# Optimization experiments

Hardware: AMD Instinct MI355X
Metric: run time of the kernel (lower is better)

## Reference

```python
import jax, jax.numpy as jnp
import numpy as np

B, Q, KV = 4, 256, 1024
QS, KS, H, VS = 128, 128, 128, 256

def setup_inputs() -> dict:
    key = jax.random.key(0)
    ks = jax.random.split(key, 7)
    return {
        "queries": jax.random.normal(ks[0], (B, Q, QS), dtype=jnp.float32),
        "keys": jax.random.normal(ks[1], (B, KV, KS), dtype=jnp.float32),
        "values": jax.random.normal(ks[2], (B, KV, VS), dtype=jnp.float32),
        "valid_lens": jax.random.randint(ks[3], (B,), 0, KV, dtype=jnp.int64 if jax.config.read('jax_enable_x64') else jnp.int32),
        "Wq": jax.random.normal(ks[4], (QS, H), dtype=jnp.float32),
        "Wk": jax.random.normal(ks[5], (KS, H), dtype=jnp.float32),
        "wv": jax.random.normal(ks[6], (H,), dtype=jnp.float32),
    }

def reference(queries, keys, values, valid_lens, Wq, Wk, wv):
    # project: [B,Q,H], [B,KV,H]
    q = jnp.einsum('bqd,dh->bqh', queries, Wq)
    k = jnp.einsum('bkd,dh->bkh', keys, Wk)
    # additive scores: broadcast add -> tanh -> reduce with w_v  [B,Q,KV]
    feats = jnp.tanh(q[:, :, None, :] + k[:, None, :, :])  # [B,Q,KV,H]
    scores = jnp.einsum('bqkh,h->bqk', feats, wv)
    # masked softmax over KV with value -1e6 at masked slots
    mask = jnp.arange(scores.shape[-1])[None, None, :] < valid_lens[:, None, None]
    scores = jnp.where(mask, scores, -1e6)
    attn = jax.nn.softmax(scores, axis=-1)
    # weighted sum of values  [B,Q,VS]
    return jnp.einsum('bqk,bkv->bqv', attn, values)
```

## Files before the change

kernel.cpp:

```cpp
#include <hip/hip_runtime.h>

#define C2LOG2E 2.8853900817779268f
#define LOG2E   1.4426950408889634f

__device__ __forceinline__ float sig2(float x) {
    return __builtin_amdgcn_rcpf(__builtin_amdgcn_exp2f(x) + 1.0f);
}

__global__ __launch_bounds__(256) void proj_kernel(
    const float* __restrict__ q_in, const float* __restrict__ k_in,
    const float* __restrict__ Wq, const float* __restrict__ Wk,
    const int* __restrict__ valid_lens,
    float* __restrict__ qc, float* __restrict__ kct)
{
    __shared__ __align__(16) float x_s[8][128];
    __shared__ __align__(16) float ps[4][8][128];
    int tid = threadIdx.x;
    int blk = blockIdx.x;
    bool is_q = (blk < 128);
    int r0 = (is_q ? blk : blk - 128) * 8;
    int bb = r0 >> 10;
    if (!is_q) {
        int vl = valid_lens[bb];
        if ((r0 & 1023) >= vl) return;
    }
    const float* X = (is_q ? q_in : k_in) + (size_t)r0 * 128;
    const float* W = is_q ? Wq : Wk;

    *(float4*)&x_s[tid >> 5][(tid & 31) * 4] = ((const float4*)X)[tid];
    __syncthreads();

    int hl = tid & 63;
    int dq = tid >> 6;
    float a0[8] = {0,0,0,0,0,0,0,0};
    float a1[8] = {0,0,0,0,0,0,0,0};
#pragma unroll
    for (int i4 = 0; i4 < 8; ++i4) {
        int d = dq*32 + i4*4;
        float w00 = W[(d+0)*128 + hl], w01 = W[(d+0)*128 + hl + 64];
        float w10 = W[(d+1)*128 + hl], w11 = W[(d+1)*128 + hl + 64];
        float w20 = W[(d+2)*128 + hl], w21 = W[(d+2)*128 + hl + 64];
        float w30 = W[(d+3)*128 + hl], w31 = W[(d+3)*128 + hl + 64];
#pragma unroll
        for (int r = 0; r < 8; ++r) {
            float4 xv = *(const float4*)&x_s[r][d];
            a0[r] = fmaf(xv.x,w00, fmaf(xv.y,w10, fmaf(xv.z,w20, fmaf(xv.w,w30, a0[r]))));
            a1[r] = fmaf(xv.x,w01, fmaf(xv.y,w11, fmaf(xv.z,w21, fmaf(xv.w,w31, a1[r]))));
        }
    }
#pragma unroll
    for (int r = 0; r < 8; ++r) {
        ps[dq][r][hl]      = a0[r];
        ps[dq][r][hl + 64] = a1[r];
    }
    __syncthreads();

    int r  = tid >> 5;
    int c4 = (tid & 31) * 4;
    float4 s0 = *(const float4*)&ps[0][r][c4];
    float4 s1 = *(const float4*)&ps[1][r][c4];
    float4 s2 = *(const float4*)&ps[2][r][c4];
    float4 s3 = *(const float4*)&ps[3][r][c4];
    float4 v = make_float4(((s0.x+s1.x)+(s2.x+s3.x))*C2LOG2E,
                           ((s0.y+s1.y)+(s2.y+s3.y))*C2LOG2E,
                           ((s0.z+s1.z)+(s2.z+s3.z))*C2LOG2E,
                           ((s0.w+s1.w)+(s2.w+s3.w))*C2LOG2E);
    if (is_q) {
        *(float4*)&qc[(size_t)(r0 + r)*128 + c4] = v;
    } else {
        int c    = (r0 & 1023) >> 6;
        int kvin = (r0 & 63) + r;
        *(float4*)&kct[((((size_t)(bb*16 + c))*32 + (c4 >> 2))*64 + kvin)*4] = v;
    }
}

__global__ __launch_bounds__(512, 4) void attn_kernel(
    const float* __restrict__ qc, const float* __restrict__ kct,
    const float* __restrict__ values, const int* __restrict__ valid_lens,
    const float* __restrict__ wv, float* __restrict__ out)
{
    __shared__ float2 e2_s[1024];
    __shared__ float4 po[8][2][64];
    __shared__ float2 red_m[8], red_s[8];

    int tid  = threadIdx.x;
    int b    = blockIdx.y;
    int q0   = blockIdx.x * 2;
    int w    = tid >> 6;
    int lane = tid & 63;
    int vl   = valid_lens[b];

    const float4* qa4 = (const float4*)(qc + (size_t)(b*256 + q0)*128);
    const float4* qb4 = qa4 + 32;
    const float4* wv4 = (const float4*)wv;
    const float4* kb  = (const float4*)kct;
    const float4* p0  = kb + ((size_t)(b*16 + w))*2048 + lane;
    const float4* p1  = p0 + 8*2048;

    bool act0 = (w*64 < vl);
    bool act1 = ((w + 8)*64 < vl);
    float a00=0.f, a10=0.f, a01=0.f, a11=0.f;

    if (act1) {
        for (int hb = 0; hb < 32; ++hb) {
            float4 wvv = wv4[hb];
            float4 qa = qa4[hb], qb = qb4[hb];
            float4 k0 = p0[(size_t)hb*64];
            float4 k1 = p1[(size_t)hb*64];
            a00 = fmaf(wvv.x, sig2(qa.x + k0.x), a00);
            a10 = fmaf(wvv.x, sig2(qb.x + k0.x), a10);
            a01 = fmaf(wvv.x, sig2(qa.x + k1.x), a01);
            a11 = fmaf(wvv.x, sig2(qb.x + k1.x), a11);
            a00 = fmaf(wvv.y, sig2(qa.y + k0.y), a00);
            a10 = fmaf(wvv.y, sig2(qb.y + k0.y), a10);
            a01 = fmaf(wvv.y, sig2(qa.y + k1.y), a01);
            a11 = fmaf(wvv.y, sig2(qb.y + k1.y), a11);
            a00 = fmaf(wvv.z, sig2(qa.z + k0.z), a00);
            a10 = fmaf(wvv.z, sig2(qb.z + k0.z), a10);
            a01 = fmaf(wvv.z, sig2(qa.z + k1.z), a01);
            a11 = fmaf(wvv.z, sig2(qb.z + k1.z), a11);
            a00 = fmaf(wvv.w, sig2(qa.w + k0.w), a00);
            a10 = fmaf(wvv.w, sig2(qb.w + k0.w), a10);
            a01 = fmaf(wvv.w, sig2(qa.w + k1.w), a01);
            a11 = fmaf(wvv.w, sig2(qb.w + k1.w), a11);
        }
    } else if (act0) {
        for (int hb = 0; hb < 32; ++hb) {
            float4 wvv = wv4[hb];
            float4 qa = qa4[hb], qb = qb4[hb];
            float4 k0 = p0[(size_t)hb*64];
            a00 = fmaf(wvv.x, sig2(qa.x + k0.x), a00);
            a10 = fmaf(wvv.x, sig2(qb.x + k0.x), a10);
            a00 = fmaf(wvv.y, sig2(qa.y + k0.y), a00);
            a10 = fmaf(wvv.y, sig2(qb.y + k0.y), a10);
            a00 = fmaf(wvv.z, sig2(qa.z + k0.z), a00);
            a10 = fmaf(wvv.z, sig2(qb.z + k0.z), a10);
            a00 = fmaf(wvv.w, sig2(qa.w + k0.w), a00);
            a10 = fmaf(wvv.w, sig2(qb.w + k0.w), a10);
        }
    }

    int kv0 = w*64 + lane, kv1 = kv0 + 512;
    bool m0v = (kv0 < vl), m1v = (kv1 < vl);
    float s00 = m0v ? -2.f*a00 : -1e6f;
    float s10 = m0v ? -2.f*a10 : -1e6f;
    float s01 = m1v ? -2.f*a01 : -1e6f;
    float s11 = m1v ? -2.f*a11 : -1e6f;

    float m0 = fmaxf(s00, s01), m1 = fmaxf(s10, s11);
#pragma unroll
    for (int off = 32; off; off >>= 1) {
        m0 = fmaxf(m0, __shfl_xor(m0, off));
        m1 = fmaxf(m1, __shfl_xor(m1, off));
    }
    if (lane == 0) red_m[w] = make_float2(m0, m1);
    __syncthreads();
    {
        float2 mm = red_m[0];
#pragma unroll
        for (int ww = 1; ww < 8; ++ww) {
            float2 t = red_m[ww];
            mm.x = fmaxf(mm.x, t.x); mm.y = fmaxf(mm.y, t.y);
        }
        m0 = mm.x; m1 = mm.y;
    }

    float e00 = __builtin_amdgcn_exp2f((s00 - m0) * LOG2E);
    float e10 = __builtin_amdgcn_exp2f((s10 - m1) * LOG2E);
    float e01 = __builtin_amdgcn_exp2f((s01 - m0) * LOG2E);
    float e11 = __builtin_amdgcn_exp2f((s11 - m1) * LOG2E);
    e2_s[kv0] = make_float2(e00, e10);
    e2_s[kv1] = make_float2(e01, e11);
    float l0 = e00 + e01, l1 = e10 + e11;
#pragma unroll
    for (int off = 32; off; off >>= 1) {
        l0 += __shfl_xor(l0, off);
        l1 += __shfl_xor(l1, off);
    }
    if (lane == 0) red_s[w] = make_float2(l0, l1);
    __syncthreads();

    int kv_end = (vl == 0) ? 1024 : vl;
    float4 ac0 = {0,0,0,0}, ac1 = {0,0,0,0};
    const float4* V4 = (const float4*)values + (size_t)b*65536 + lane;
#pragma unroll 2
    for (int k2 = w; k2 < kv_end; k2 += 8) {
        float4 vv = V4[(size_t)k2*64];
        float2 ee = e2_s[k2];
        ac0.x = fmaf(ee.x, vv.x, ac0.x); ac0.y = fmaf(ee.x, vv.y, ac0.y);
        ac0.z = fmaf(ee.x, vv.z, ac0.z); ac0.w = fmaf(ee.x, vv.w, ac0.w);
        ac1.x = fmaf(ee.y, vv.x, ac1.x); ac1.y = fmaf(ee.y, vv.y, ac1.y);
        ac1.z = fmaf(ee.y, vv.z, ac1.z); ac1.w = fmaf(ee.y, vv.w, ac1.w);
    }
    po[w][0][lane] = ac0;
    po[w][1][lane] = ac1;
    __syncthreads();

    int qq  = tid >> 8;
    int col = tid & 255;
    float ssum = 0.f;
#pragma unroll
    for (int ww = 0; ww < 8; ++ww) {
        float2 t = red_s[ww];
        ssum += qq ? t.y : t.x;
    }
    const float* pp = (const float*)po;
    float r = 0.f;
#pragma unroll
    for (int ww = 0; ww < 8; ++ww) r += pp[(ww*2 + qq)*256 + col];
    out[((size_t)(b*256 + q0 + qq))*256 + col] = r / ssum;
}

extern "C" void kernel_launch(void* const* d_in, const int* in_sizes, int n_in,
                              void* d_out, int out_size, void* d_ws, size_t ws_size,
                              hipStream_t stream)
{
    const float* queries = (const float*)d_in[0];
    const float* keys    = (const float*)d_in[1];
    const float* values  = (const float*)d_in[2];
    const int*   vlens   = (const int*)d_in[3];
    const float* Wq      = (const float*)d_in[4];
    const float* Wk      = (const float*)d_in[5];
    const float* wv      = (const float*)d_in[6];
    float* out = (float*)d_out;

    float* qc  = (float*)d_ws;
    float* kct = qc + 4*256*128;

    proj_kernel<<<640, 256, 0, stream>>>(queries, keys, Wq, Wk, vlens, qc, kct);
    attn_kernel<<<dim3(128, 4), 512, 0, stream>>>(qc, kct, values, vlens, wv, out);
}
```

Before: 99.62 us.

## Split attention KV range across two blocks with flash-decoding style combine

Splits the KV dimension into two halves handled by separate blocks (grid z=2), each writing partial outputs plus max/sum statistics to workspace, followed by a new combine kernel that rescales and merges them. This doubles block count and halves per-block register/LDS use (launch bounds raised to 8 waves per SIMD hint), improving occupancy and load balance when valid lengths vary. It adds an extra kernel launch and a round trip of partial outputs through global memory.

```diff
diff --git a/kernel.cpp b/kernel.cpp
--- a/kernel.cpp
+++ b/kernel.cpp
@@ -74,57 +74,37 @@
     }
 }
 
-__global__ __launch_bounds__(512, 4) void attn_kernel(
+__global__ __launch_bounds__(512, 8) void attn_split_kernel(
     const float* __restrict__ qc, const float* __restrict__ kct,
     const float* __restrict__ values, const int* __restrict__ valid_lens,
-    const float* __restrict__ wv, float* __restrict__ out)
-{
-    __shared__ float2 e2_s[1024];
+    const float* __restrict__ wv, float* __restrict__ pO, float* __restrict__ pml)
+{
+    __shared__ float2 e2_s[512];
     __shared__ float4 po[8][2][64];
     __shared__ float2 red_m[8], red_s[8];
 
     int tid  = threadIdx.x;
     int b    = blockIdx.y;
     int q0   = blockIdx.x * 2;
+    int s    = blockIdx.z;
     int w    = tid >> 6;
     int lane = tid & 63;
     int vl   = valid_lens[b];
-
-    const float4* qa4 = (const float4*)(qc + (size_t)(b*256 + q0)*128);
+    int row0 = b*256 + q0;
+
+    if (s == 1 && vl > 0 && vl <= 512) {
+        if (tid < 2) pml[(size_t)(1024 + row0 + tid)*2] = -1e30f;
+        return;
+    }
+
+    const float4* qa4 = (const float4*)(qc + (size_t)row0*128);
     const float4* qb4 = qa4 + 32;
     const float4* wv4 = (const float4*)wv;
-    const float4* kb  = (const float4*)kct;
-    const float4* p0  = kb + ((size_t)(b*16 + w))*2048 + lane;
-    const float4* p1  = p0 + 8*2048;
-
-    bool act0 = (w*64 < vl);
-    bool act1 = ((w + 8)*64 < vl);
-    float a00=0.f, a10=0.f, a01=0.f, a11=0.f;
-
-    if (act1) {
-        for (int hb = 0; hb < 32; ++hb) {
-            float4 wvv = wv4[hb];
-            float4 qa = qa4[hb], qb = qb4[hb];
-            float4 k0 = p0[(size_t)hb*64];
-            float4 k1 = p1[(size_t)hb*64];
-            a00 = fmaf(wvv.x, sig2(qa.x + k0.x), a00);
-            a10 = fmaf(wvv.x, sig2(qb.x + k0.x), a10);
-            a01 = fmaf(wvv.x, sig2(qa.x + k1.x), a01);
-            a11 = fmaf(wvv.x, sig2(qb.x + k1.x), a11);
-            a00 = fmaf(wvv.y, sig2(qa.y + k0.y), a00);
-            a10 = fmaf(wvv.y, sig2(qb.y + k0.y), a10);
-            a01 = fmaf(wvv.y, sig2(qa.y + k1.y), a01);
-            a11 = fmaf(wvv.y, sig2(qb.y + k1.y), a11);
-            a00 = fmaf(wvv.z, sig2(qa.z + k0.z), a00);
-            a10 = fmaf(wvv.z, sig2(qb.z + k0.z), a10);
-            a01 = fmaf(wvv.z, sig2(qa.z + k1.z), a01);
-            a11 = fmaf(wvv.z, sig2(qb.z + k1.z), a11);
-            a00 = fmaf(wvv.w, sig2(qa.w + k0.w), a00);
-            a10 = fmaf(wvv.w, sig2(qb.w + k0.w), a10);
-            a01 = fmaf(wvv.w, sig2(qa.w + k1.w), a01);
-            a11 = fmaf(wvv.w, sig2(qb.w + k1.w), a11);
-        }
-    } else if (act0) {
+    const float4* p0  = (const float4*)kct + ((size_t)(b*16 + s*8 + w))*2048 + lane;
+
+    float a00 = 0.f, a10 = 0.f;
+    if ((s*8 + w)*64 < vl) {
+#pragma unroll 4
         for (int hb = 0; hb < 32; ++hb) {
             float4 wvv = wv4[hb];
             float4 qa = qa4[hb], qb = qb4[hb];
@@ -140,14 +120,12 @@
         }
     }
 
-    int kv0 = w*64 + lane, kv1 = kv0 + 512;
-    bool m0v = (kv0 < vl), m1v = (kv1 < vl);
-    float s00 = m0v ? -2.f*a00 : -1e6f;
-    float s10 = m0v ? -2.f*a10 : -1e6f;
-    float s01 = m1v ? -2.f*a01 : -1e6f;
-    float s11 = m1v ? -2.f*a11 : -1e6f;
-
-    float m0 = fmaxf(s00, s01), m1 = fmaxf(s10, s11);
+    int lkv = w*64 + lane;
+    bool valid = (s*512 + lkv < vl);
+    float s00 = valid ? -2.f*a00 : -1e6f;
+    float s10 = valid ? -2.f*a10 : -1e6f;
+
+    float m0 = s00, m1 = s10;
 #pragma unroll
     for (int off = 32; off; off >>= 1) {
         m0 = fmaxf(m0, __shfl_xor(m0, off));
@@ -167,11 +145,8 @@
 
     float e00 = __builtin_amdgcn_exp2f((s00 - m0) * LOG2E);
     float e10 = __builtin_amdgcn_exp2f((s10 - m1) * LOG2E);
-    float e01 = __builtin_amdgcn_exp2f((s01 - m0) * LOG2E);
-    float e11 = __builtin_amdgcn_exp2f((s11 - m1) * LOG2E);
-    e2_s[kv0] = make_float2(e00, e10);
-    e2_s[kv1] = make_float2(e01, e11);
-    float l0 = e00 + e01, l1 = e10 + e11;
+    e2_s[lkv] = make_float2(e00, e10);
+    float l0 = e00, l1 = e10;
 #pragma unroll
     for (int off = 32; off; off >>= 1) {
         l0 += __shfl_xor(l0, off);
@@ -180,11 +155,11 @@
     if (lane == 0) red_s[w] = make_float2(l0, l1);
     __syncthreads();
 
-    int kv_end = (vl == 0) ? 1024 : vl;
+    int local_end = (vl == 0) ? 512 : min(512, vl - s*512);
     float4 ac0 = {0,0,0,0}, ac1 = {0,0,0,0};
-    const float4* V4 = (const float4*)values + (size_t)b*65536 + lane;
+    const float4* V4 = (const float4*)values + (size_t)b*65536 + (size_t)s*512*64 + lane;
 #pragma unroll 2
-    for (int k2 = w; k2 < kv_end; k2 += 8) {
+    for (int k2 = w; k2 < local_end; k2 += 8) {
         float4 vv = V4[(size_t)k2*64];
         float2 ee = e2_s[k2];
         ac0.x = fmaf(ee.x, vv.x, ac0.x); ac0.y = fmaf(ee.x, vv.y, ac0.y);
@@ -194,21 +169,49 @@
     }
     po[w][0][lane] = ac0;
     po[w][1][lane] = ac1;
+
+    if (tid < 2) {
+        float lsum = 0.f;
+#pragma unroll
+        for (int ww = 0; ww < 8; ++ww) {
+            float2 t = red_s[ww];
+            lsum += tid ? t.y : t.x;
+        }
+        float mm = tid ? m1 : m0;
+        *(float2*)&pml[(size_t)(s*1024 + row0 + tid)*2] = make_float2(mm, lsum);
+    }
     __syncthreads();
 
     int qq  = tid >> 8;
     int col = tid & 255;
-    float ssum = 0.f;
-#pragma unroll
-    for (int ww = 0; ww < 8; ++ww) {
-        float2 t = red_s[ww];
-        ssum += qq ? t.y : t.x;
-    }
     const float* pp = (const float*)po;
     float r = 0.f;
 #pragma unroll
     for (int ww = 0; ww < 8; ++ww) r += pp[(ww*2 + qq)*256 + col];
-    out[((size_t)(b*256 + q0 + qq))*256 + col] = r / ssum;
+    pO[(size_t)(s*1024 + row0 + qq)*256 + col] = r;
+}
+
+__global__ __launch_bounds__(256) void combine_kernel(
+    const float* __restrict__ pO, const float* __restrict__ pml,
+    float* __restrict__ out)
+{
+    int tid  = threadIdx.x;
+    int row  = blockIdx.x*4 + (tid >> 6);
+    int lane = tid & 63;
+    float2 ml0 = *(const float2*)&pml[(size_t)row*2];
+    float2 ml1 = *(const float2*)&pml[(size_t)(1024 + row)*2];
+    float m  = fmaxf(ml0.x, ml1.x);
+    float w0 = __builtin_amdgcn_exp2f((ml0.x - m) * LOG2E);
+    float w1 = __builtin_amdgcn_exp2f((ml1.x - m) * LOG2E);
+    float inv = 1.0f / (w0*ml0.y + w1*ml1.y);
+    float4 o0 = ((const float4*)pO)[(size_t)row*64 + lane];
+    float4 o1 = ((const float4*)pO)[(size_t)(1024 + row)*64 + lane];
+    float4 o;
+    o.x = (w0*o0.x + w1*o1.x) * inv;
+    o.y = (w0*o0.y + w1*o1.y) * inv;
+    o.z = (w0*o0.z + w1*o1.z) * inv;
+    o.w = (w0*o0.w + w1*o1.w) * inv;
+    ((float4*)out)[(size_t)row*64 + lane] = o;
 }
 
 extern "C" void kernel_launch(void* const* d_in, const int* in_sizes, int n_in,
@@ -225,8 +228,11 @@
     float* out = (float*)d_out;
 
     float* qc  = (float*)d_ws;
-    float* kct = qc + 4*256*128;
+    float* kct = qc  + 4*256*128;
+    float* pO  = kct + 4*16*32*64*4;
+    float* pml = pO  + 2*1024*256;
 
     proj_kernel<<<640, 256, 0, stream>>>(queries, keys, Wq, Wk, vlens, qc, kct);
-    attn_kernel<<<dim3(128, 4), 512, 0, stream>>>(qc, kct, values, vlens, wv, out);
-}
+    attn_split_kernel<<<dim3(128, 4, 2), 512, 0, stream>>>(qc, kct, values, vlens, wv, pO, pml);
+    combine_kernel<<<256, 256, 0, stream>>>(pO, pml, out);
+}
```

Result: faster. 95.08 us, median of 2 (-4.6%).
